# Kernel optimization log

Hardware: AMD Instinct MI355X
Metric: run time of the kernel (lower is better)

The kernel has to match this reference:

```python
import jax, jax.numpy as jnp
import numpy as np

C_IN, LAT, OUT, EMB = 3, 64, 512, 5
B, H = 128, 128
KS = [4, 4, 3, 4, 2]                       # per-layer dynamic kernel sizes
CHANS = [C_IN, LAT, LAT * 2, LAT * 4, LAT * 8]  # in-channels of each dyn conv
MIX = [(C_IN, LAT), (LAT, LAT * 2), (LAT * 2, LAT * 4), (LAT * 4, LAT * 8), (LAT * 8, OUT)]


def setup_inputs() -> dict:
    key = jax.random.key(0)
    ks = jax.random.split(key, 40)
    nrm = lambda k, shape, s=0.02: jax.random.normal(k, shape, jnp.float32) * s
    inp = {}
    inp["input"] = jax.random.normal(ks[0], (B, C_IN, H, H), jnp.float32)
    inp["label"] = jax.random.randint(ks[1], (B,), 0, 10)
    inp["emb"] = nrm(ks[2], (10, EMB), 1.0)  # label embedding table
    i = 3
    for j, (c, k) in enumerate(zip(CHANS, KS), 1):  # label -> dyn kernel linears
        inp[f"l{j}_w"] = nrm(ks[i], (EMB, c * k * k), 0.1)
        inp[f"l{j}_b"] = jnp.zeros((c * k * k,), jnp.float32)
        i += 1
    for j, (ci, co) in enumerate(MIX, 1):  # channel-mixer linears
        inp[f"cm{j}_w"] = nrm(ks[i], (ci, co))
        inp[f"cm{j}_b"] = jnp.zeros((co,), jnp.float32)
        i += 1
    for j, c in enumerate([LAT, LAT * 2, LAT * 4, LAT * 8], 1):  # BN affine params
        inp[f"bn{j}_g"] = jnp.ones((c,), jnp.float32)
        inp[f"bn{j}_b"] = jnp.zeros((c,), jnp.float32)
    return inp


def dw_conv(x, k, stride, pad):
    """Per-sample, per-channel (depthwise) 2d cross-correlation.
    x: (B,C,H,W), k: (B,C,h,w) -> (B,C,H',W')."""
    def one(xi, ki):
        return jax.lax.conv_general_dilated(
            xi[None], ki[:, None], (stride, stride),
            [(pad, pad), (pad, pad)],
            dimension_numbers=("NCHW", "OIHW", "NCHW"),
            feature_group_count=xi.shape[0])[0]
    return jax.vmap(one)(x, k)


def reference(input, label, emb,
              l1_w, l1_b, l2_w, l2_b, l3_w, l3_b, l4_w, l4_b, l5_w, l5_b,
              cm1_w, cm1_b, cm2_w, cm2_b, cm3_w, cm3_b, cm4_w, cm4_b, cm5_w, cm5_b,
              bn1_g, bn1_b, bn2_g, bn2_b, bn3_g, bn3_b, bn4_g, bn4_b):
    e = emb[label]  # (B, EMB)
    dk = lambda w, b, c, k: jnp.tanh(e @ w + b).reshape(-1, c, k, k)
    k1 = dk(l1_w, l1_b, C_IN, 4)
    k2 = dk(l2_w, l2_b, LAT, 4)
    k3 = dk(l3_w, l3_b, LAT * 2, 3)
    k4 = dk(l4_w, l4_b, LAT * 4, 4)
    k5 = dk(l5_w, l5_b, LAT * 8, 2)

    mix = lambda z, w, b: jnp.einsum("bchw,cd->bdhw", z, w) + b[None, :, None, None]
    lrelu = lambda z: jax.nn.leaky_relu(z, 0.2)

    def bn(z, g, b):  # training-mode BN (batch statistics, biased var, eps=1e-5)
        m = z.mean((0, 2, 3), keepdims=True)
        v = z.var((0, 2, 3), keepdims=True)
        return (z - m) * jax.lax.rsqrt(v + 1e-5) * g[None, :, None, None] + b[None, :, None, None]

    z = bn(lrelu(mix(dw_conv(input, k1, 2, 1), cm1_w, cm1_b)), bn1_g, bn1_b)
    z = bn(lrelu(mix(dw_conv(z, k2, 2, 1), cm2_w, cm2_b)), bn2_g, bn2_b)
    z = bn(lrelu(mix(dw_conv(z, k3, 2, 1), cm3_w, cm3_b)), bn3_g, bn3_b)
    z = bn(lrelu(mix(dw_conv(z, k4, 2, 1), cm4_w, cm4_b)), bn4_g, bn4_b)
    z = jax.nn.sigmoid(mix(dw_conv(z, k5, 1, 0), cm5_w, cm5_b))  # (B, OUT, 7, 7)
    return (z, label)
```

## Files before the change

### kernel.cpp

```cpp
#include <hip/hip_runtime.h>
#include <hip/hip_bf16.h>

typedef __hip_bfloat16 bf16;
using short8  = __attribute__((ext_vector_type(8))) short;
using floatx4 = __attribute__((ext_vector_type(4))) float;

__device__ __forceinline__ float b2f(unsigned short u) {
    union { unsigned int i; float f; } v; v.i = ((unsigned int)u) << 16; return v.f;
}
__device__ __forceinline__ unsigned short f2b(float f) {
    bf16 h = __float2bfloat16(f);
    return *(unsigned short*)&h;
}

#define NREP 16

__global__ __launch_bounds__(256) void prep_kernel(
    const int* __restrict__ label, const float* __restrict__ emb,
    const float* __restrict__ l1w, const float* __restrict__ l1b,
    const float* __restrict__ l2w, const float* __restrict__ l2b,
    const float* __restrict__ l3w, const float* __restrict__ l3b,
    const float* __restrict__ l4w, const float* __restrict__ l4b,
    const float* __restrict__ l5w, const float* __restrict__ l5b,
    float* __restrict__ dynk, float* __restrict__ stats,
    float* __restrict__ labelOut)
{
    const int tid = threadIdx.x;
    if (blockIdx.x == gridDim.x - 1) {
        for (int i = tid; i < 30720; i += 256) stats[i] = 0.0f;
        if (tid < 128) labelOut[tid] = (float)label[tid];
        return;
    }
    int idx = blockIdx.x * 256 + tid;
    if (idx >= 1071104) return;
    const float* w; const float* bb; int loc, ckk, ksk, base;
    if (idx < 6144)        { w = l1w; bb = l1b; loc = idx;          ckk = 48;   ksk = 0;  base = 0;      }
    else if (idx < 137216) { w = l2w; bb = l2b; loc = idx - 6144;   ckk = 1024; ksk = 16; base = 6144;   }
    else if (idx < 284672) { w = l3w; bb = l3b; loc = idx - 137216; ckk = 1152; ksk = 9;  base = 137216; }
    else if (idx < 808960) { w = l4w; bb = l4b; loc = idx - 284672; ckk = 4096; ksk = 16; base = 284672; }
    else                   { w = l5w; bb = l5b; loc = idx - 808960; ckk = 2048; ksk = 4;  base = 808960; }
    int b   = loc / ckk;
    int col = loc - b * ckk;
    int lab = label[b];
    float acc = bb[col];
    #pragma unroll
    for (int m = 0; m < 5; ++m)
        acc = fmaf(emb[lab * 5 + m], w[m * ckk + col], acc);
    float val = tanhf(acc);
    if (ksk == 0) {
        dynk[idx] = val;
    } else {
        int c  = col / ksk;
        int t  = col - c * ksk;
        int Cl = ckk / ksk;
        dynk[base + b * ckk + t * Cl + c] = val;
    }
}

__global__ void bn_prep(const float* __restrict__ st,
                        const float* __restrict__ gam, const float* __restrict__ bet,
                        float* __restrict__ aff, int C, float NINV)
{
    int c = threadIdx.x;
    if (c >= C) return;
    float s = 0.f, q = 0.f;
    #pragma unroll
    for (int r = 0; r < NREP; ++r) {
        s += st[r * 2 * C + c];
        q += st[r * 2 * C + C + c];
    }
    float m   = s * NINV;
    float var = fmaf(q, NINV, -m * m);
    float sc  = gam[c] * rsqrtf(var + 1e-5f);
    aff[c]     = sc;
    aff[C + c] = fmaf(-m, sc, bet[c]);
}

__global__ __launch_bounds__(256) void wt_kernel(
    const float* __restrict__ w2, const float* __restrict__ w3,
    const float* __restrict__ w4, const float* __restrict__ w5,
    bf16* __restrict__ wt2, bf16* __restrict__ wt3,
    bf16* __restrict__ wt4, bf16* __restrict__ wt5)
{
    __shared__ float T[32][33];
    const int tid = threadIdx.x;
    int t = blockIdx.x;
    const float* W; bf16* WT; int K, N, tl;
    if (t < 8)        { W = w2; WT = wt2; K = 64;  N = 128; tl = t; }
    else if (t < 40)  { W = w3; WT = wt3; K = 128; N = 256; tl = t - 8; }
    else if (t < 168) { W = w4; WT = wt4; K = 256; N = 512; tl = t - 40; }
    else              { W = w5; WT = wt5; K = 512; N = 512; tl = t - 168; }
    const int NT = N >> 5;
    const int kt = tl / NT, nt = tl - kt * NT;
    const int k0 = kt * 32, n0 = nt * 32;
    const int cc = tid & 31, rr = tid >> 5;
    #pragma unroll
    for (int it = 0; it < 4; ++it) {
        int k = rr + it * 8;
        T[k][cc] = W[(long)(k0 + k) * N + n0 + cc];
    }
    __syncthreads();
    #pragma unroll
    for (int it = 0; it < 4; ++it) {
        int n = rr + it * 8;
        WT[(long)(n0 + n) * K + k0 + cc] = __float2bfloat16(T[cc][n]);
    }
}

__global__ __launch_bounds__(256) void fused_l1_v6(
    const float* __restrict__ xf, const float* __restrict__ dynk,
    const float* __restrict__ W, const float* __restrict__ bias,
    bf16* __restrict__ y, float* __restrict__ statsOut)
{
    constexpr int HIN = 128, HOUT = 64;
    constexpr int TW = 32, TH = 8;
    constexpr int PS  = 68;
    constexpr int PCH = 18 * PS;

    __shared__ float patch[3 * PCH];
    __shared__ __align__(16) float dwT[32 * 28];
    __shared__ float Wlds[192];
    __shared__ float klds[48];
    __shared__ float biasL[64];
    __shared__ float sums[64], sqs[64];

    const int tid = threadIdx.x;
    const int b   = blockIdx.x >> 4;
    const int tl  = blockIdx.x & 15;
    const int ty0 = (tl >> 1) * TH;
    const int tx0 = (tl & 1) * TW;

    if (tid < 48) klds[tid] = dynk[b * 48 + tid];
    if (tid >= 64 && tid < 256) Wlds[tid - 64] = W[tid - 64];
    if (tid < 64) { biasL[tid] = bias[tid]; sums[tid] = 0.f; sqs[tid] = 0.f; }

    {
        const int iy0 = ty0 * 2 - 1, ix0 = tx0 * 2 - 1;
        #pragma unroll
        for (int k = 0; k < 15; ++k) {
            int i  = tid + k * 256;
            int c  = i / 1224;
            int r  = i - c * 1224;
            int py = r / 68, px = r - py * 68;
            int gy = iy0 + py, gx = ix0 + px;
            bool slot = (i < 3672);
            bool inb  = slot && (px < 66) &&
                        ((unsigned)gy < (unsigned)HIN) && ((unsigned)gx < (unsigned)HIN);
            float v = 0.f;
            if (inb) v = xf[((long)b * 3 + c) * (HIN * HIN) + gy * HIN + gx];
            if (slot) patch[c * PCH + py * PS + px] = v;
        }
    }
    __syncthreads();

    {
        const int py = tid >> 5, px = tid & 31;
        const int pixg = tid >> 3, j = tid & 7;
        #pragma unroll
        for (int c = 0; c < 3; ++c) {
            const float* pb = &patch[c * PCH + (py * 2) * PS + px * 2];
            float a = 0.f;
            #pragma unroll
            for (int kh = 0; kh < 4; ++kh)
                #pragma unroll
                for (int kw = 0; kw < 4; ++kw)
                    a = fmaf(pb[kh * PS + kw], klds[c * 16 + kh * 4 + kw], a);
            dwT[pixg * 28 + j * 3 + c] = a;
        }
    }
    __syncthreads();

    {
        const int cq = tid & 7, pixg = tid >> 3;
        const int d0 = cq * 8;
        float Wr[3][8], bi[8];
        #pragma unroll
        for (int c = 0; c < 3; ++c)
            #pragma unroll
            for (int t = 0; t < 8; ++t) Wr[c][t] = Wlds[c * 64 + d0 + t];
        #pragma unroll
        for (int t = 0; t < 8; ++t) bi[t] = biasL[d0 + t];

        float dv[24];
        #pragma unroll
        for (int q4 = 0; q4 < 6; ++q4)
            *(float4*)&dv[q4 * 4] = *(const float4*)&dwT[pixg * 28 + q4 * 4];

        float sreg[8] = {}, qreg[8] = {};
        #pragma unroll
        for (int j = 0; j < 8; ++j) {
            const int pos = pixg * 8 + j;
            const float dv0 = dv[j * 3 + 0];
            const float dv1 = dv[j * 3 + 1];
            const float dv2 = dv[j * 3 + 2];
            const int py = pos >> 5, px = pos & 31;
            const long row = ((long)(b * HOUT + ty0 + py)) * HOUT + tx0 + px;
            union { uint4 v; unsigned short us[8]; } pk;
            #pragma unroll
            for (int t = 0; t < 8; ++t) {
                float v = fmaf(dv0, Wr[0][t], fmaf(dv1, Wr[1][t], fmaf(dv2, Wr[2][t], bi[t])));
                v = v > 0.f ? v : 0.2f * v;
                sreg[t] += v;
                qreg[t] = fmaf(v, v, qreg[t]);
                pk.us[t] = f2b(v);
            }
            *(uint4*)&y[row * 64 + d0] = pk.v;
        }
        #pragma unroll
        for (int m = 8; m < 64; m <<= 1)
            #pragma unroll
            for (int t = 0; t < 8; ++t) {
                sreg[t] += __shfl_xor(sreg[t], m);
                qreg[t] += __shfl_xor(qreg[t], m);
            }
        if ((tid & 63) < 8) {
            #pragma unroll
            for (int t = 0; t < 8; ++t) {
                atomicAdd(&sums[d0 + t], sreg[t]);
                atomicAdd(&sqs [d0 + t], qreg[t]);
            }
        }
    }
    __syncthreads();
    {
        const int rep = blockIdx.x & (NREP - 1);
        if (tid < 64) {
            atomicAdd(&statsOut[rep * 128 + tid],      sums[tid]);
            atomicAdd(&statsOut[rep * 128 + 64 + tid], sqs[tid]);
        }
    }
}

template<int C, int KS, int HIN, int HOUT, int STRIDE, int PAD, int NTHR>
__global__ __launch_bounds__(NTHR) void dw_direct(
    const bf16* __restrict__ x, const float* __restrict__ aff,
    const float* __restrict__ dynkT, bf16* __restrict__ outA)
{
    constexpr int G   = C / 8;
    constexpr int KSK = KS * KS;
    static_assert(NTHR == HOUT * G, "one output row per block");

    __shared__ __align__(16) float wlds[KSK * C];

    const int tid = threadIdx.x;
    const int b   = blockIdx.x / HOUT;
    const int oy  = blockIdx.x % HOUT;

    {
        const float* src = dynkT + (long)b * (KSK * C);
        for (int i = tid * 4; i < KSK * C; i += NTHR * 4)
            *(float4*)&wlds[i] = *(const float4*)&src[i];
    }
    __syncthreads();

    const int g  = tid % G;
    const int ox = tid / G;
    const int c0 = g * 8;
    const int iy0 = oy * STRIDE - PAD;
    const int ix0 = ox * STRIDE - PAD;

    float sc[8], sh[8];
    {
        float4 a0 = *(const float4*)&aff[c0];
        float4 a1 = *(const float4*)&aff[c0 + 4];
        float4 b0 = *(const float4*)&aff[C + c0];
        float4 b1 = *(const float4*)&aff[C + c0 + 4];
        sc[0]=a0.x; sc[1]=a0.y; sc[2]=a0.z; sc[3]=a0.w;
        sc[4]=a1.x; sc[5]=a1.y; sc[6]=a1.z; sc[7]=a1.w;
        sh[0]=b0.x; sh[1]=b0.y; sh[2]=b0.z; sh[3]=b0.w;
        sh[4]=b1.x; sh[5]=b1.y; sh[6]=b1.z; sh[7]=b1.w;
    }

    float acc[8];
    #pragma unroll
    for (int ch = 0; ch < 8; ++ch) acc[ch] = 0.f;

    const bool interior = (iy0 >= 0) && (iy0 + KS <= HIN) &&
                          (ix0 >= 0) && (ix0 + KS <= HIN);

    if (interior) {
        const bf16* bp = x + ((long)(b * HIN + iy0) * HIN + ix0) * C + c0;
        uint4 v[KSK];
        #pragma unroll
        for (int kh = 0; kh < KS; ++kh)
            #pragma unroll
            for (int kw = 0; kw < KS; ++kw)
                v[kh * KS + kw] = *(const uint4*)(bp + (kh * HIN + kw) * C);
        #pragma unroll
        for (int t = 0; t < KSK; ++t) {
            const float* wp = &wlds[t * C + c0];
            float4 wa = *(const float4*)wp;
            float4 wb = *(const float4*)(wp + 4);
            const float wt[8] = {wa.x, wa.y, wa.z, wa.w, wb.x, wb.y, wb.z, wb.w};
            #pragma unroll
            for (int ch = 0; ch < 8; ++ch) {
                unsigned u = ((const unsigned*)&v[t])[ch >> 1];
                unsigned bits = (ch & 1) ? (u & 0xffff0000u) : (u << 16);
                float xb = fmaf(__uint_as_float(bits), sc[ch], sh[ch]);
                acc[ch] = fmaf(xb, wt[ch], acc[ch]);
            }
        }
    } else {
        #pragma unroll
        for (int kh = 0; kh < KS; ++kh) {
            const int iy = iy0 + kh;
            if ((unsigned)iy >= (unsigned)HIN) continue;
            #pragma unroll
            for (int kw = 0; kw < KS; ++kw) {
                const int ix = ix0 + kw;
                if ((unsigned)ix >= (unsigned)HIN) continue;
                uint4 v = *(const uint4*)&x[((long)(b * HIN + iy) * HIN + ix) * C + c0];
                const float* wp = &wlds[(kh * KS + kw) * C + c0];
                float4 wa = *(const float4*)wp;
                float4 wb = *(const float4*)(wp + 4);
                const float wt[8] = {wa.x, wa.y, wa.z, wa.w, wb.x, wb.y, wb.z, wb.w};
                #pragma unroll
                for (int ch = 0; ch < 8; ++ch) {
                    unsigned u = ((const unsigned*)&v)[ch >> 1];
                    unsigned bits = (ch & 1) ? (u & 0xffff0000u) : (u << 16);
                    float xb = fmaf(__uint_as_float(bits), sc[ch], sh[ch]);
                    acc[ch] = fmaf(xb, wt[ch], acc[ch]);
                }
            }
        }
    }

    union { uint4 v; unsigned short us[8]; } pk;
    #pragma unroll
    for (int ch = 0; ch < 8; ++ch) pk.us[ch] = f2b(acc[ch]);
    *(uint4*)&outA[((long)(b * HOUT + oy) * HOUT + ox) * C + c0] = pk.v;
}

template<int K, int COUT, bool LAST>
__global__ __launch_bounds__(256) void gemm_layer(
    const bf16* __restrict__ A, const bf16* __restrict__ WT,
    const float* __restrict__ bias, bf16* __restrict__ y,
    float* __restrict__ statsOut, float* __restrict__ outF, int Mtiles)
{
    constexpr int SK = 72;
    constexpr int CS = 136;
    __shared__ __align__(16) unsigned short smem[18432];
    unsigned short* As  = smem;
    unsigned short* Bs  = smem + 9216;
    unsigned short* Csh = smem;
    __shared__ float sums[128], sqs[128];

    const int tid  = threadIdx.x;
    const int lane = tid & 63;
    const int w    = tid >> 6;
    const int wm   = (w >> 1) * 64, wn = (w & 1) * 64;
    const int lm   = lane & 15, lq = lane >> 4;
    const int mt   = blockIdx.x % Mtiles;
    const int nt   = blockIdx.x / Mtiles;
    const long m0  = (long)mt * 128;
    const int  n0  = nt * 128;

    floatx4 acc[4][4];
    #pragma unroll
    for (int i = 0; i < 4; ++i)
        #pragma unroll
        for (int j = 0; j < 4; ++j) acc[i][j] = (floatx4)0.0f;

    for (int kb = 0; kb < K; kb += 64) {
        __syncthreads();
        #pragma unroll
        for (int s = 0; s < 4; ++s) {
            int i = tid + s * 256;
            int m = i >> 3, q = i & 7;
            uint4 va = *(const uint4*)(A  + ((m0 + m) * K + kb + q * 8));
            uint4 vb = *(const uint4*)(WT + ((long)(n0 + m) * K + kb + q * 8));
            *(uint4*)&As[m * SK + q * 8] = va;
            *(uint4*)&Bs[m * SK + q * 8] = vb;
        }
        __syncthreads();
        #pragma unroll
        for (int h = 0; h < 2; ++h) {
            short8 af[4], bfr[4];
            #pragma unroll
            for (int i = 0; i < 4; ++i) {
                af[i]  = *(const short8*)&As[(wm + i * 16 + lm) * SK + h * 32 + lq * 8];
                bfr[i] = *(const short8*)&Bs[(wn + i * 16 + lm) * SK + h * 32 + lq * 8];
            }
            #pragma unroll
            for (int i = 0; i < 4; ++i)
                #pragma unroll
                for (int j = 0; j < 4; ++j)
                    acc[i][j] = __builtin_amdgcn_mfma_f32_16x16x32_bf16(af[i], bfr[j], acc[i][j], 0, 0, 0);
        }
    }
    __syncthreads();

    float bj[4];
    #pragma unroll
    for (int j = 0; j < 4; ++j) bj[j] = bias[n0 + wn + j * 16 + lm];

    if constexpr (!LAST) {
        if (tid < 128) { sums[tid] = 0.f; sqs[tid] = 0.f; }
        #pragma unroll
        for (int i = 0; i < 4; ++i)
            #pragma unroll
            for (int j = 0; j < 4; ++j) {
                int c = wn + j * 16 + lm;
                #pragma unroll
                for (int rg = 0; rg < 4; ++rg) {
                    int r = wm + i * 16 + lq * 4 + rg;
                    float v = acc[i][j][rg] + bj[j];
                    v = v > 0.f ? v : 0.2f * v;
                    Csh[r * CS + c] = f2b(v);
                }
            }
        __syncthreads();
        const int cg = tid & 15, mr = tid >> 4;
        float sacc[8], qacc[8];
        #pragma unroll
        for (int t = 0; t < 8; ++t) { sacc[t] = 0.f; qacc[t] = 0.f; }
        #pragma unroll
        for (int it = 0; it < 8; ++it) {
            int m = mr + it * 16;
            uint4 pk = *(const uint4*)&Csh[m * CS + cg * 8];
            *(uint4*)&y[(m0 + m) * COUT + n0 + cg * 8] = pk;
            const unsigned short* pu = (const unsigned short*)&pk;
            #pragma unroll
            for (int t = 0; t < 8; ++t) {
                float f = b2f(pu[t]);
                sacc[t] += f;
                qacc[t] = fmaf(f, f, qacc[t]);
            }
        }
        #pragma unroll
        for (int t = 0; t < 8; ++t) {
            atomicAdd(&sums[cg * 8 + t], sacc[t]);
            atomicAdd(&sqs [cg * 8 + t], qacc[t]);
        }
        __syncthreads();
        {
            const int rep = blockIdx.x & (NREP - 1);
            if (tid < 128) {
                atomicAdd(&statsOut[rep * 2 * COUT + n0 + tid],        sums[tid]);
                atomicAdd(&statsOut[rep * 2 * COUT + COUT + n0 + tid], sqs[tid]);
            }
        }
    } else {
        #pragma unroll
        for (int i = 0; i < 4; ++i)
            #pragma unroll
            for (int j = 0; j < 4; ++j) {
                int c  = wn + j * 16 + lm;
                int rb = wm + i * 16 + lq * 4;
                ushort4 pk;
                unsigned short* pp = (unsigned short*)&pk;
                #pragma unroll
                for (int rg = 0; rg < 4; ++rg)
                    pp[rg] = f2b(acc[i][j][rg] + bj[j]);
                *(ushort4*)&Csh[c * CS + rb] = pk;
            }
        __syncthreads();
        const int mg = tid & 15, nr = tid >> 4;
        #pragma unroll
        for (int it = 0; it < 8; ++it) {
            int n = nr + it * 16;
            uint4 pk = *(const uint4*)&Csh[n * CS + mg * 8];
            const unsigned short* pu = (const unsigned short*)&pk;
            #pragma unroll
            for (int t = 0; t < 8; ++t) {
                int m = (int)m0 + mg * 8 + t;
                int b = m / 49, pos = m - b * 49;
                float v = b2f(pu[t]);
                outF[((long)(b * 512 + n0 + n)) * 49 + pos] = 1.f / (1.f + __expf(-v));
            }
        }
    }
}


extern "C" void kernel_launch(void* const* d_in, const int* in_sizes, int n_in,
                              void* d_out, int out_size, void* d_ws, size_t ws_size,
                              hipStream_t stream)
{
    const float* input = (const float*)d_in[0];
    const int*   label = (const int*)d_in[1];
    const float* emb   = (const float*)d_in[2];
    const float* lw[5] = {(const float*)d_in[3], (const float*)d_in[5], (const float*)d_in[7],
                          (const float*)d_in[9], (const float*)d_in[11]};
    const float* lb[5] = {(const float*)d_in[4], (const float*)d_in[6], (const float*)d_in[8],
                          (const float*)d_in[10], (const float*)d_in[12]};
    const float* cmw[5] = {(const float*)d_in[13], (const float*)d_in[15], (const float*)d_in[17],
                           (const float*)d_in[19], (const float*)d_in[21]};
    const float* cmb[5] = {(const float*)d_in[14], (const float*)d_in[16], (const float*)d_in[18],
                           (const float*)d_in[20], (const float*)d_in[22]};
    const float* bng[4] = {(const float*)d_in[23], (const float*)d_in[25],
                           (const float*)d_in[27], (const float*)d_in[29]};
    const float* bnb[4] = {(const float*)d_in[24], (const float*)d_in[26],
                           (const float*)d_in[28], (const float*)d_in[30]};
    float* out = (float*)d_out;

    float* wsf   = (float*)d_ws;
    float* dynk  = wsf;
    float* stats = wsf + 1071104;
    const float* k1  = dynk;
    const float* k2T = dynk + 6144;
    const float* k3T = dynk + 137216;
    const float* k4T = dynk + 284672;
    const float* k5T = dynk + 808960;
    float* st1 = stats;
    float* st2 = stats + 2048;
    float* st3 = stats + 6144;
    float* st4 = stats + 14336;

    bf16* wt  = (bf16*)((char*)d_ws + 4407296);
    bf16* wt2 = wt;
    bf16* wt3 = wt + 8192;
    bf16* wt4 = wt + 40960;
    bf16* wt5 = wt + 172032;
    bf16* S1  = (bf16*)((char*)d_ws + 5308416);
    bf16* S2  = (bf16*)((char*)d_ws + 72417280);
    float* affBase = (float*)((char*)d_ws + 89194496);
    float* aff1 = affBase;
    float* aff2 = affBase + 128;
    float* aff3 = affBase + 384;
    float* aff4 = affBase + 896;

    prep_kernel<<<4186, 256, 0, stream>>>(label, emb,
        lw[0], lb[0], lw[1], lb[1], lw[2], lb[2], lw[3], lb[3], lw[4], lb[4],
        dynk, stats, out + 3211264);
    wt_kernel<<<424, 256, 0, stream>>>(cmw[1], cmw[2], cmw[3], cmw[4],
                                       wt2, wt3, wt4, wt5);

    fused_l1_v6<<<2048, 256, 0, stream>>>(input, k1, cmw[0], cmb[0], S1, st1);

    bn_prep<<<1, 64, 0, stream>>>(st1, bng[0], bnb[0], aff1, 64, 1.f / 524288.f);
    dw_direct<64, 4, 64, 32, 2, 1, 256><<<4096, 256, 0, stream>>>(S1, aff1, k2T, S2);
    gemm_layer<64, 128, false><<<1024, 256, 0, stream>>>(
        S2, wt2, cmb[1], S1, st2, nullptr, 1024);

    bn_prep<<<1, 128, 0, stream>>>(st2, bng[1], bnb[1], aff2, 128, 1.f / 131072.f);
    dw_direct<128, 3, 32, 16, 2, 1, 256><<<2048, 256, 0, stream>>>(S1, aff2, k3T, S2);
    gemm_layer<128, 256, false><<<512, 256, 0, stream>>>(
        S2, wt3, cmb[2], S1, st3, nullptr, 256);

    bn_prep<<<1, 256, 0, stream>>>(st3, bng[2], bnb[2], aff3, 256, 1.f / 32768.f);
    dw_direct<256, 4, 16, 8, 2, 1, 256><<<1024, 256, 0, stream>>>(S1, aff3, k4T, S2);
    gemm_layer<256, 512, false><<<256, 256, 0, stream>>>(
        S2, wt4, cmb[3], S1, st4, nullptr, 64);

    bn_prep<<<1, 512, 0, stream>>>(st4, bng[3], bnb[3], aff4, 512, 1.f / 8192.f);
    dw_direct<512, 2, 8, 7, 1, 0, 448><<<896, 448, 0, stream>>>(S1, aff4, k5T, S2);
    gemm_layer<512, 512, true><<<196, 256, 0, stream>>>(
        S2, wt5, cmb[4], nullptr, nullptr, out, 49);
}
```

Baseline: 327.1 us.

## Fuse layer-2 depthwise conv into channel-mix GEMM with BN stats

Adds a gemm2_fused kernel that computes the layer-2 BN-affine plus depthwise 4x4 stride-2 conv directly into the GEMM's shared-memory A tile. It then runs the MFMA channel mix, leaky-ReLU, output store and BN statistics in the same kernel. This removes the separate dw_direct launch and the round trip of its intermediate activation through global memory. Buffer assignments for later layers are changed to distinct regions so layers no longer ping-pong between S1 and S2. The cost is redundant overlapping input reads per block and more register pressure from 16 uint4 loads per thread.

After: 324.9 us. Within noise of the previous version (-0.7%).

```diff
diff --git a/kernel.cpp b/kernel.cpp
--- a/kernel.cpp
+++ b/kernel.cpp
@@ -227,6 +227,160 @@
         if (tid < 64) {
             atomicAdd(&statsOut[rep * 128 + tid],      sums[tid]);
             atomicAdd(&statsOut[rep * 128 + 64 + tid], sqs[tid]);
+        }
+    }
+}
+
+__global__ __launch_bounds__(256) void gemm2_fused(
+    const bf16* __restrict__ y1, const bf16* __restrict__ WT,
+    const float* __restrict__ aff, const float* __restrict__ k2T,
+    const float* __restrict__ bias, bf16* __restrict__ y,
+    float* __restrict__ statsOut)
+{
+    constexpr int SK = 72;
+    constexpr int CS = 136;
+    __shared__ __align__(16) unsigned short smem[18432];
+    unsigned short* As  = smem;
+    unsigned short* Bs  = smem + 9216;
+    unsigned short* Csh = smem;
+    __shared__ float klds[1024];
+    __shared__ float scL[64], shL[64];
+    __shared__ float sums[128], sqs[128];
+
+    const int tid  = threadIdx.x;
+    const int lane = tid & 63;
+    const int w    = tid >> 6;
+    const int wm   = (w >> 1) * 64, wn = (w & 1) * 64;
+    const int lm   = lane & 15, lq = lane >> 4;
+    const long m0  = (long)blockIdx.x * 128;
+    const int  b   = (int)(m0 >> 10);
+
+    *(float4*)&klds[tid * 4] = *(const float4*)&k2T[b * 1024 + tid * 4];
+    if (tid < 64) { scL[tid] = aff[tid]; shL[tid] = aff[64 + tid]; }
+    #pragma unroll
+    for (int s = 0; s < 4; ++s) {
+        int i = tid + s * 256;
+        int n = i >> 3, q = i & 7;
+        uint4 vb = *(const uint4*)(WT + (long)n * 64 + q * 8);
+        *(uint4*)&Bs[n * SK + q * 8] = vb;
+    }
+    __syncthreads();
+
+    #pragma unroll
+    for (int s = 0; s < 4; ++s) {
+        int i = tid + s * 256;
+        int m = i >> 3, q = i & 7;
+        int pos = (int)((m0 + m) & 1023);
+        int oy = pos >> 5, ox = pos & 31;
+        int c0 = q * 8;
+        int iy0 = oy * 2 - 1, ix0 = ox * 2 - 1;
+
+        float sc[8], sh[8];
+        #pragma unroll
+        for (int ch = 0; ch < 8; ++ch) { sc[ch] = scL[c0 + ch]; sh[ch] = shL[c0 + ch]; }
+
+        uint4 v[16];
+        #pragma unroll
+        for (int t = 0; t < 16; ++t) {
+            int iy = iy0 + (t >> 2), ix = ix0 + (t & 3);
+            int iyc = min(max(iy, 0), 63), ixc = min(max(ix, 0), 63);
+            v[t] = *(const uint4*)&y1[((long)(b * 64 + iyc) * 64 + ixc) * 64 + c0];
+        }
+        float acc[8];
+        #pragma unroll
+        for (int ch = 0; ch < 8; ++ch) acc[ch] = 0.f;
+        #pragma unroll
+        for (int t = 0; t < 16; ++t) {
+            int iy = iy0 + (t >> 2), ix = ix0 + (t & 3);
+            bool ok = ((unsigned)iy < 64u) && ((unsigned)ix < 64u);
+            float4 wa = *(const float4*)&klds[t * 64 + c0];
+            float4 wb = *(const float4*)&klds[t * 64 + c0 + 4];
+            const float wt[8] = {wa.x, wa.y, wa.z, wa.w, wb.x, wb.y, wb.z, wb.w};
+            #pragma unroll
+            for (int ch = 0; ch < 8; ++ch) {
+                unsigned u = ((const unsigned*)&v[t])[ch >> 1];
+                unsigned bits = (ch & 1) ? (u & 0xffff0000u) : (u << 16);
+                float xb = ok ? fmaf(__uint_as_float(bits), sc[ch], sh[ch]) : 0.f;
+                acc[ch] = fmaf(xb, wt[ch], acc[ch]);
+            }
+        }
+        union { uint4 u4; unsigned short us[8]; } pk;
+        #pragma unroll
+        for (int ch = 0; ch < 8; ++ch) pk.us[ch] = f2b(acc[ch]);
+        *(uint4*)&As[m * SK + q * 8] = pk.u4;
+    }
+    __syncthreads();
+
+    floatx4 acc[4][4];
+    #pragma unroll
+    for (int i = 0; i < 4; ++i)
+        #pragma unroll
+        for (int j = 0; j < 4; ++j) acc[i][j] = (floatx4)0.0f;
+    #pragma unroll
+    for (int h = 0; h < 2; ++h) {
+        short8 af[4], bfr[4];
+        #pragma unroll
+        for (int i = 0; i < 4; ++i) {
+            af[i]  = *(const short8*)&As[(wm + i * 16 + lm) * SK + h * 32 + lq * 8];
+            bfr[i] = *(const short8*)&Bs[(wn + i * 16 + lm) * SK + h * 32 + lq * 8];
+        }
+        #pragma unroll
+        for (int i = 0; i < 4; ++i)
+            #pragma unroll
+            for (int j = 0; j < 4; ++j)
+                acc[i][j] = __builtin_amdgcn_mfma_f32_16x16x32_bf16(af[i], bfr[j], acc[i][j], 0, 0, 0);
+    }
+    __syncthreads();
+
+    float bj[4];
+    #pragma unroll
+    for (int j = 0; j < 4; ++j) bj[j] = bias[wn + j * 16 + lm];
+
+    if (tid < 128) { sums[tid] = 0.f; sqs[tid] = 0.f; }
+    #pragma unroll
+    for (int i = 0; i < 4; ++i)
+        #pragma unroll
+        for (int j = 0; j < 4; ++j) {
+            int c = wn + j * 16 + lm;
+            #pragma unroll
+            for (int rg = 0; rg < 4; ++rg) {
+                int r = wm + i * 16 + lq * 4 + rg;
+                float v = acc[i][j][rg] + bj[j];
+                v = v > 0.f ? v : 0.2f * v;
+                Csh[r * CS + c] = f2b(v);
+            }
+        }
+    __syncthreads();
+    {
+        const int cg = tid & 15, mr = tid >> 4;
+        float sacc[8], qacc[8];
+        #pragma unroll
+        for (int t = 0; t < 8; ++t) { sacc[t] = 0.f; qacc[t] = 0.f; }
+        #pragma unroll
+        for (int it = 0; it < 8; ++it) {
+            int m = mr + it * 16;
+            uint4 pk = *(const uint4*)&Csh[m * CS + cg * 8];
+            *(uint4*)&y[(m0 + m) * 128 + cg * 8] = pk;
+            const unsigned short* pu = (const unsigned short*)&pk;
+            #pragma unroll
+            for (int t = 0; t < 8; ++t) {
+                float f = b2f(pu[t]);
+                sacc[t] += f;
+                qacc[t] = fmaf(f, f, qacc[t]);
+            }
+        }
+        #pragma unroll
+        for (int t = 0; t < 8; ++t) {
+            atomicAdd(&sums[cg * 8 + t], sacc[t]);
+            atomicAdd(&sqs [cg * 8 + t], qacc[t]);
+        }
+    }
+    __syncthreads();
+    {
+        const int rep = blockIdx.x & (NREP - 1);
+        if (tid < 128) {
+            atomicAdd(&statsOut[rep * 256 + tid],        sums[tid]);
+            atomicAdd(&statsOut[rep * 256 + 128 + tid],  sqs[tid]);
         }
     }
 }
@@ -514,11 +668,17 @@
     bf16* wt5 = wt + 172032;
     bf16* S1  = (bf16*)((char*)d_ws + 5308416);
     bf16* S2  = (bf16*)((char*)d_ws + 72417280);
-    float* affBase = (float*)((char*)d_ws + 89194496);
+    float* affBase = (float*)((char*)d_ws + 105971712);
     float* aff1 = affBase;
     float* aff2 = affBase + 128;
     float* aff3 = affBase + 384;
     float* aff4 = affBase + 896;
+
+    bf16* A3 = S1;
+    bf16* y3 = S1 + 4194304;
+    bf16* A4 = S1 + 12582912;
+    bf16* y4 = S1 + 14680064;
+    bf16* A5 = S1 + 18874368;
 
     prep_kernel<<<4186, 256, 0, stream>>>(label, emb,
         lw[0], lb[0], lw[1], lb[1], lw[2], lb[2], lw[3], lb[3], lw[4], lb[4],
@@ -529,22 +689,20 @@
     fused_l1_v6<<<2048, 256, 0, stream>>>(input, k1, cmw[0], cmb[0], S1, st1);
 
     bn_prep<<<1, 64, 0, stream>>>(st1, bng[0], bnb[0], aff1, 64, 1.f / 524288.f);
-    dw_direct<64, 4, 64, 32, 2, 1, 256><<<4096, 256, 0, stream>>>(S1, aff1, k2T, S2);
-    gemm_layer<64, 128, false><<<1024, 256, 0, stream>>>(
-        S2, wt2, cmb[1], S1, st2, nullptr, 1024);
+    gemm2_fused<<<1024, 256, 0, stream>>>(S1, wt2, aff1, k2T, cmb[1], S2, st2);
 
     bn_prep<<<1, 128, 0, stream>>>(st2, bng[1], bnb[1], aff2, 128, 1.f / 131072.f);
-    dw_direct<128, 3, 32, 16, 2, 1, 256><<<2048, 256, 0, stream>>>(S1, aff2, k3T, S2);
+    dw_direct<128, 3, 32, 16, 2, 1, 256><<<2048, 256, 0, stream>>>(S2, aff2, k3T, A3);
     gemm_layer<128, 256, false><<<512, 256, 0, stream>>>(
-        S2, wt3, cmb[2], S1, st3, nullptr, 256);
+        A3, wt3, cmb[2], y3, st3, nullptr, 256);
 
     bn_prep<<<1, 256, 0, stream>>>(st3, bng[2], bnb[2], aff3, 256, 1.f / 32768.f);
-    dw_direct<256, 4, 16, 8, 2, 1, 256><<<1024, 256, 0, stream>>>(S1, aff3, k4T, S2);
+    dw_direct<256, 4, 16, 8, 2, 1, 256><<<1024, 256, 0, stream>>>(y3, aff3, k4T, A4);
     gemm_layer<256, 512, false><<<256, 256, 0, stream>>>(
-        S2, wt4, cmb[3], S1, st4, nullptr, 64);
+        A4, wt4, cmb[3], y4, st4, nullptr, 64);
 
     bn_prep<<<1, 512, 0, stream>>>(st4, bng[3], bnb[3], aff4, 512, 1.f / 8192.f);
-    dw_direct<512, 2, 8, 7, 1, 0, 448><<<896, 448, 0, stream>>>(S1, aff4, k5T, S2);
+    dw_direct<512, 2, 8, 7, 1, 0, 448><<<896, 448, 0, stream>>>(y4, aff4, k5T, A5);
     gemm_layer<512, 512, true><<<196, 256, 0, stream>>>(
-        S2, wt5, cmb[4], nullptr, nullptr, out, 49);
-}
+        A5, wt5, cmb[4], nullptr, nullptr, out, 49);
+}
```
